# Performance work log

Measured on AMD Instinct MI355X. Metric: run time of the kernel, lower is better.

## Reference

```python
import jax, jax.numpy as jnp
import numpy as np

COND = 128  # mask = first 128 dims are condition (True); last 128 are transformed


def _mlp(h, W1, b1, W2, b2, W3, b3):
    h = jax.nn.relu(h @ W1 + b1)
    h = jax.nn.relu(h @ W2 + b2)
    return h @ W3 + b3


def setup_inputs() -> dict:
    key = jax.random.key(0)
    ks = jax.random.split(key, 8)
    B, D, H, T = 65536, 256, 512, 128
    s = 0.02  # small init so exp(tanh(s_vals)) is well-behaved
    inp = {
        "x": jax.random.normal(ks[0], (B, D), dtype=jnp.float32),
        "Ws1": jax.random.normal(ks[1], (COND, H), dtype=jnp.float32) * s,
        "bs1": jnp.zeros((H,), jnp.float32),
        "Ws2": jax.random.normal(ks[2], (H, H), dtype=jnp.float32) * s,
        "bs2": jnp.zeros((H,), jnp.float32),
        "Ws3": jax.random.normal(ks[3], (H, T), dtype=jnp.float32) * s,
        "bs3": jnp.zeros((T,), jnp.float32),
        "Wt1": jax.random.normal(ks[4], (COND, H), dtype=jnp.float32) * s,
        "bt1": jnp.zeros((H,), jnp.float32),
        "Wt2": jax.random.normal(ks[5], (H, H), dtype=jnp.float32) * s,
        "bt2": jnp.zeros((H,), jnp.float32),
        "Wt3": jax.random.normal(ks[6], (H, T), dtype=jnp.float32) * s,
        "bt3": jnp.zeros((T,), jnp.float32),
    }
    return inp


def reference(x, Ws1, bs1, Ws2, bs2, Ws3, bs3, Wt1, bt1, Wt2, bt2, Wt3, bt3):
    # mask gather: condition = masked dims, transform = the rest
    cond = x[:, :COND]            # [B, COND]
    x_t = x[:, COND:]             # [B, T]
    s_vals = jnp.tanh(_mlp(cond, Ws1, bs1, Ws2, bs2, Ws3, bs3))  # [B, T]
    t_vals = _mlp(cond, Wt1, bt1, Wt2, bt2, Wt3, bt3)            # [B, T]
    y_partial = x_t * jnp.exp(s_vals) + t_vals                   # forward branch (inverse=False)
    log_det = s_vals.sum(axis=1)                                 # [B]
    y = jnp.concatenate([cond, y_partial], axis=1)               # scatter back
    return (y, log_det)
```

## Files before the change

### kernel.cpp

```cpp
#include <hip/hip_runtime.h>
#include <hip/hip_bf16.h>

typedef __bf16          bf16x8_t __attribute__((ext_vector_type(8)));
typedef float           f32x4_t  __attribute__((ext_vector_type(4)));
typedef unsigned short  u16x4_t  __attribute__((ext_vector_type(4)));

#define DIN      256
#define CONDN    128
#define BM       64
#define NTHREADS 512
#define NWAVE    8
#define LDA      136
#define LDH      520

#define OFF_WS1 0
#define OFF_WS2 65536
#define OFF_WS3 327680
#define OFF_WT1 393216
#define OFF_WT2 458752
#define OFF_WT3 720896
#define W_TOTAL 786432

__global__ void prep_w(const float* __restrict__ Ws1, const float* __restrict__ Ws2,
                       const float* __restrict__ Ws3, const float* __restrict__ Wt1,
                       const float* __restrict__ Wt2, const float* __restrict__ Wt3,
                       __hip_bfloat16* __restrict__ wt) {
  int idx = blockIdx.x * blockDim.x + threadIdx.x;
  if (idx >= W_TOTAL) return;
  const float* W; int K, N, off;
  if (idx < OFF_WS2)      { W = Ws1; K = 128; N = 512; off = idx - OFF_WS1; }
  else if (idx < OFF_WS3) { W = Ws2; K = 512; N = 512; off = idx - OFF_WS2; }
  else if (idx < OFF_WT1) { W = Ws3; K = 512; N = 128; off = idx - OFF_WS3; }
  else if (idx < OFF_WT2) { W = Wt1; K = 128; N = 512; off = idx - OFF_WT1; }
  else if (idx < OFF_WT3) { W = Wt2; K = 512; N = 512; off = idx - OFF_WT2; }
  else                    { W = Wt3; K = 512; N = 128; off = idx - OFF_WT3; }
  int n = off / K;
  int k = off - n * K;
  wt[idx] = __float2bfloat16(W[k * N + n]);
}

template<int KTOT, int MT, int NT>
__device__ __forceinline__ void mm_tile(const __hip_bfloat16* __restrict__ Asrc, const int lda,
                                        const __hip_bfloat16* __restrict__ Bsrc,
                                        const int l15, const int l4, f32x4_t acc[MT][NT]) {
  #pragma unroll 4
  for (int kk = 0; kk < KTOT; kk += 32) {
    bf16x8_t a[MT], b[NT];
    #pragma unroll
    for (int m = 0; m < MT; ++m)
      a[m] = *reinterpret_cast<const bf16x8_t*>(&Asrc[(m * 16 + l15) * lda + kk + l4 * 8]);
    #pragma unroll
    for (int n = 0; n < NT; ++n)
      b[n] = *reinterpret_cast<const bf16x8_t*>(&Bsrc[(n * 16 + l15) * KTOT + kk + l4 * 8]);
    #pragma unroll
    for (int m = 0; m < MT; ++m) {
      #pragma unroll
      for (int n = 0; n < NT; ++n)
        acc[m][n] = __builtin_amdgcn_mfma_f32_16x16x32_bf16(a[m], b[n], acc[m][n], 0, 0, 0);
    }
  }
}

template<int MT, int NT>
__device__ __forceinline__ void relu_store(f32x4_t acc[MT][NT], const float* __restrict__ bias,
                                           const int n0, const int l15, const int l4,
                                           __hip_bfloat16* __restrict__ H) {
  #pragma unroll
  for (int n = 0; n < NT; ++n) {
    const float bv = bias[n0 + n * 16 + l15];
    #pragma unroll
    for (int m = 0; m < MT; ++m) {
      #pragma unroll
      for (int r = 0; r < 4; ++r) {
        float v = acc[m][n][r] + bv;
        v = fmaxf(v, 0.0f);
        H[(m * 16 + l4 * 4 + r) * LDH + n0 + n * 16 + l15] = __float2bfloat16(v);
      }
    }
  }
}

#define ZERO_ACC(acc, MT, NT) do {                       \
    _Pragma("unroll") for (int m_ = 0; m_ < MT; ++m_)    \
    _Pragma("unroll") for (int n_ = 0; n_ < NT; ++n_)    \
      acc[m_][n_] = (f32x4_t){0.f, 0.f, 0.f, 0.f};       \
  } while (0)

__global__ __launch_bounds__(NTHREADS, 2)
void realnvp_fused(const float* __restrict__ x, const __hip_bfloat16* __restrict__ wt,
                   const float* __restrict__ bs1, const float* __restrict__ bs2,
                   const float* __restrict__ bs3, const float* __restrict__ bt1,
                   const float* __restrict__ bt2, const float* __restrict__ bt3,
                   float* __restrict__ y, float* __restrict__ ld) {
  __shared__ __hip_bfloat16 sA[BM * LDA];
  __shared__ __hip_bfloat16 sH1[BM * LDH];
  __shared__ __hip_bfloat16 sH2[BM * LDH];
  __shared__ float sLd[NWAVE][BM];

  const int tid  = threadIdx.x;
  const int lane = tid & 63;
  const int wid  = tid >> 6;
  const int l15  = lane & 15;
  const int l4   = lane >> 4;
  const int row0 = blockIdx.x * BM;
  const int n0   = wid * 64;
  const int n3   = wid * 16;

  #pragma unroll
  for (int i = 0; i < 4; ++i) {
    int f = tid + i * NTHREADS;
    int r = f >> 5;
    int c = (f & 31) << 2;
    const float4 v = *reinterpret_cast<const float4*>(&x[(size_t)(row0 + r) * DIN + c]);
    *reinterpret_cast<float4*>(&y[(size_t)(row0 + r) * DIN + c]) = v;
    union { u16x4_t u; __hip_bfloat16 b[4]; } p;
    p.b[0] = __float2bfloat16(v.x); p.b[1] = __float2bfloat16(v.y);
    p.b[2] = __float2bfloat16(v.z); p.b[3] = __float2bfloat16(v.w);
    *reinterpret_cast<u16x4_t*>(&sA[r * LDA + c]) = p.u;
  }
  __syncthreads();

  f32x4_t acc[4][4];
  f32x4_t sfrag[4], tfrag[4];

  ZERO_ACC(acc, 4, 4);
  mm_tile<128, 4, 4>(sA, LDA, wt + OFF_WS1 + (size_t)n0 * 128, l15, l4, acc);
  relu_store<4, 4>(acc, bs1, n0, l15, l4, sH1);
  __syncthreads();
  ZERO_ACC(acc, 4, 4);
  mm_tile<512, 4, 4>(sH1, LDH, wt + OFF_WS2 + (size_t)n0 * 512, l15, l4, acc);
  relu_store<4, 4>(acc, bs2, n0, l15, l4, sH2);
  __syncthreads();
  {
    f32x4_t a3[4][1];
    ZERO_ACC(a3, 4, 1);
    mm_tile<512, 4, 1>(sH2, LDH, wt + OFF_WS3 + (size_t)n3 * 512, l15, l4, a3);
    #pragma unroll
    for (int m = 0; m < 4; ++m) sfrag[m] = a3[m][0];
  }

  ZERO_ACC(acc, 4, 4);
  mm_tile<128, 4, 4>(sA, LDA, wt + OFF_WT1 + (size_t)n0 * 128, l15, l4, acc);
  relu_store<4, 4>(acc, bt1, n0, l15, l4, sH1);
  __syncthreads();
  ZERO_ACC(acc, 4, 4);
  mm_tile<512, 4, 4>(sH1, LDH, wt + OFF_WT2 + (size_t)n0 * 512, l15, l4, acc);
  relu_store<4, 4>(acc, bt2, n0, l15, l4, sH2);
  __syncthreads();
  {
    f32x4_t a3[4][1];
    ZERO_ACC(a3, 4, 1);
    mm_tile<512, 4, 1>(sH2, LDH, wt + OFF_WT3 + (size_t)n3 * 512, l15, l4, a3);
    #pragma unroll
    for (int m = 0; m < 4; ++m) tfrag[m] = a3[m][0];
  }

  const float bsv = bs3[n3 + l15];
  const float btv = bt3[n3 + l15];
  #pragma unroll
  for (int m = 0; m < 4; ++m) {
    #pragma unroll
    for (int r = 0; r < 4; ++r) {
      const int rl   = m * 16 + l4 * 4 + r;
      const int grow = row0 + rl;
      const int col  = n3 + l15;
      float s = tanhf(sfrag[m][r] + bsv);
      float t = tfrag[m][r] + btv;
      float xv = x[(size_t)grow * DIN + CONDN + col];
      y[(size_t)grow * DIN + CONDN + col] = xv * expf(s) + t;
      float ss = s;
      ss += __shfl_xor(ss, 1);
      ss += __shfl_xor(ss, 2);
      ss += __shfl_xor(ss, 4);
      ss += __shfl_xor(ss, 8);
      if (l15 == 0) sLd[wid][rl] = ss;
    }
  }
  __syncthreads();
  if (tid < BM) {
    float v = 0.f;
    #pragma unroll
    for (int w = 0; w < NWAVE; ++w) v += sLd[w][tid];
    ld[row0 + tid] = v;
  }
}

extern "C" void kernel_launch(void* const* d_in, const int* in_sizes, int n_in,
                              void* d_out, int out_size, void* d_ws, size_t ws_size,
                              hipStream_t stream) {
  const float* x   = (const float*)d_in[0];
  const float* Ws1 = (const float*)d_in[1];
  const float* bs1 = (const float*)d_in[2];
  const float* Ws2 = (const float*)d_in[3];
  const float* bs2 = (const float*)d_in[4];
  const float* Ws3 = (const float*)d_in[5];
  const float* bs3 = (const float*)d_in[6];
  const float* Wt1 = (const float*)d_in[7];
  const float* bt1 = (const float*)d_in[8];
  const float* Wt2 = (const float*)d_in[9];
  const float* bt2 = (const float*)d_in[10];
  const float* Wt3 = (const float*)d_in[11];
  const float* bt3 = (const float*)d_in[12];

  const int Btot = in_sizes[0] / DIN;
  float* y  = (float*)d_out;
  float* ld = (float*)d_out + (size_t)Btot * DIN;
  __hip_bfloat16* wt = (__hip_bfloat16*)d_ws;

  prep_w<<<(W_TOTAL + 255) / 256, 256, 0, stream>>>(Ws1, Ws2, Ws3, Wt1, Wt2, Wt3, wt);
  realnvp_fused<<<Btot / BM, NTHREADS, 0, stream>>>(x, wt, bs1, bs2, bs3,
                                                    bt1, bt2, bt3, y, ld);
}
```

Before: 234.0 us.

## Swizzle LDS, merge hidden buffers, prefetch weight fragments, raise occupancy bound

Replaces padded shared-memory layouts with an XOR swizzle and merges the two hidden-activation buffers into one, adding extra barriers so a layer's output can overwrite its input. Weight fragments from global memory are software-prefetched one k-step ahead in registers. The launch bound is raised to request more resident blocks, which shrinks the per-thread register budget and risks spilling the large accumulator arrays.

```diff
diff --git a/kernel.cpp b/kernel.cpp
--- a/kernel.cpp
+++ b/kernel.cpp
@@ -10,8 +10,6 @@
 #define BM       64
 #define NTHREADS 512
 #define NWAVE    8
-#define LDA      136
-#define LDH      520
 
 #define OFF_WS1 0
 #define OFF_WS2 65536
@@ -39,42 +37,56 @@
   wt[idx] = __float2bfloat16(W[k * N + n]);
 }
 
+#define SWZ(row, col) (((((col) >> 3) ^ ((row) & 7)) << 3) + ((col) & 7))
+
 template<int KTOT, int MT, int NT>
-__device__ __forceinline__ void mm_tile(const __hip_bfloat16* __restrict__ Asrc, const int lda,
+__device__ __forceinline__ void mm_tile(const __hip_bfloat16* __restrict__ As, const int lda,
                                         const __hip_bfloat16* __restrict__ Bsrc,
                                         const int l15, const int l4, f32x4_t acc[MT][NT]) {
-  #pragma unroll 4
+  const int xr = l15 & 7;
+  bf16x8_t a[MT], b[NT], bn[NT];
+  #pragma unroll
+  for (int n = 0; n < NT; ++n)
+    b[n] = *reinterpret_cast<const bf16x8_t*>(&Bsrc[(n * 16 + l15) * KTOT + l4 * 8]);
+  #pragma unroll
   for (int kk = 0; kk < KTOT; kk += 32) {
-    bf16x8_t a[MT], b[NT];
+    if (kk + 32 < KTOT) {
+      #pragma unroll
+      for (int n = 0; n < NT; ++n)
+        bn[n] = *reinterpret_cast<const bf16x8_t*>(&Bsrc[(n * 16 + l15) * KTOT + kk + 32 + l4 * 8]);
+    }
     #pragma unroll
     for (int m = 0; m < MT; ++m)
-      a[m] = *reinterpret_cast<const bf16x8_t*>(&Asrc[(m * 16 + l15) * lda + kk + l4 * 8]);
-    #pragma unroll
-    for (int n = 0; n < NT; ++n)
-      b[n] = *reinterpret_cast<const bf16x8_t*>(&Bsrc[(n * 16 + l15) * KTOT + kk + l4 * 8]);
+      a[m] = *reinterpret_cast<const bf16x8_t*>(
+          &As[(m * 16 + l15) * lda + ((((kk >> 3) + l4) ^ xr) << 3)]);
     #pragma unroll
     for (int m = 0; m < MT; ++m) {
       #pragma unroll
       for (int n = 0; n < NT; ++n)
         acc[m][n] = __builtin_amdgcn_mfma_f32_16x16x32_bf16(a[m], b[n], acc[m][n], 0, 0, 0);
     }
-  }
-}
-
-template<int MT, int NT>
+    if (kk + 32 < KTOT) {
+      #pragma unroll
+      for (int n = 0; n < NT; ++n) b[n] = bn[n];
+    }
+  }
+}
+
+template<int MT, int NT, int LD>
 __device__ __forceinline__ void relu_store(f32x4_t acc[MT][NT], const float* __restrict__ bias,
                                            const int n0, const int l15, const int l4,
                                            __hip_bfloat16* __restrict__ H) {
   #pragma unroll
   for (int n = 0; n < NT; ++n) {
-    const float bv = bias[n0 + n * 16 + l15];
+    const int col = n0 + n * 16 + l15;
+    const float bv = bias[col];
     #pragma unroll
     for (int m = 0; m < MT; ++m) {
       #pragma unroll
       for (int r = 0; r < 4; ++r) {
-        float v = acc[m][n][r] + bv;
-        v = fmaxf(v, 0.0f);
-        H[(m * 16 + l4 * 4 + r) * LDH + n0 + n * 16 + l15] = __float2bfloat16(v);
+        const int row = m * 16 + l4 * 4 + r;
+        float v = fmaxf(acc[m][n][r] + bv, 0.0f);
+        H[row * LD + SWZ(row, col)] = __float2bfloat16(v);
       }
     }
   }
@@ -86,16 +98,15 @@
       acc[m_][n_] = (f32x4_t){0.f, 0.f, 0.f, 0.f};       \
   } while (0)
 
-__global__ __launch_bounds__(NTHREADS, 2)
+__global__ __launch_bounds__(NTHREADS, 4)
 void realnvp_fused(const float* __restrict__ x, const __hip_bfloat16* __restrict__ wt,
                    const float* __restrict__ bs1, const float* __restrict__ bs2,
                    const float* __restrict__ bs3, const float* __restrict__ bt1,
                    const float* __restrict__ bt2, const float* __restrict__ bt3,
                    float* __restrict__ y, float* __restrict__ ld) {
-  __shared__ __hip_bfloat16 sA[BM * LDA];
-  __shared__ __hip_bfloat16 sH1[BM * LDH];
-  __shared__ __hip_bfloat16 sH2[BM * LDH];
-  __shared__ float sLd[NWAVE][BM];
+  __shared__ __hip_bfloat16 sA[BM * CONDN];
+  __shared__ __hip_bfloat16 sH[BM * 512];
+  float* sLd = reinterpret_cast<float*>(sA);
 
   const int tid  = threadIdx.x;
   const int lane = tid & 63;
@@ -116,7 +127,7 @@
     union { u16x4_t u; __hip_bfloat16 b[4]; } p;
     p.b[0] = __float2bfloat16(v.x); p.b[1] = __float2bfloat16(v.y);
     p.b[2] = __float2bfloat16(v.z); p.b[3] = __float2bfloat16(v.w);
-    *reinterpret_cast<u16x4_t*>(&sA[r * LDA + c]) = p.u;
+    *reinterpret_cast<u16x4_t*>(&sA[r * CONDN + SWZ(r, c)]) = p.u;
   }
   __syncthreads();
 
@@ -124,33 +135,36 @@
   f32x4_t sfrag[4], tfrag[4];
 
   ZERO_ACC(acc, 4, 4);
-  mm_tile<128, 4, 4>(sA, LDA, wt + OFF_WS1 + (size_t)n0 * 128, l15, l4, acc);
-  relu_store<4, 4>(acc, bs1, n0, l15, l4, sH1);
-  __syncthreads();
-  ZERO_ACC(acc, 4, 4);
-  mm_tile<512, 4, 4>(sH1, LDH, wt + OFF_WS2 + (size_t)n0 * 512, l15, l4, acc);
-  relu_store<4, 4>(acc, bs2, n0, l15, l4, sH2);
+  mm_tile<128, 4, 4>(sA, CONDN, wt + OFF_WS1 + (size_t)n0 * 128, l15, l4, acc);
+  relu_store<4, 4, 512>(acc, bs1, n0, l15, l4, sH);
+  __syncthreads();
+  ZERO_ACC(acc, 4, 4);
+  mm_tile<512, 4, 4>(sH, 512, wt + OFF_WS2 + (size_t)n0 * 512, l15, l4, acc);
+  __syncthreads();
+  relu_store<4, 4, 512>(acc, bs2, n0, l15, l4, sH);
   __syncthreads();
   {
     f32x4_t a3[4][1];
     ZERO_ACC(a3, 4, 1);
-    mm_tile<512, 4, 1>(sH2, LDH, wt + OFF_WS3 + (size_t)n3 * 512, l15, l4, a3);
+    mm_tile<512, 4, 1>(sH, 512, wt + OFF_WS3 + (size_t)n3 * 512, l15, l4, a3);
     #pragma unroll
     for (int m = 0; m < 4; ++m) sfrag[m] = a3[m][0];
   }
-
-  ZERO_ACC(acc, 4, 4);
-  mm_tile<128, 4, 4>(sA, LDA, wt + OFF_WT1 + (size_t)n0 * 128, l15, l4, acc);
-  relu_store<4, 4>(acc, bt1, n0, l15, l4, sH1);
-  __syncthreads();
-  ZERO_ACC(acc, 4, 4);
-  mm_tile<512, 4, 4>(sH1, LDH, wt + OFF_WT2 + (size_t)n0 * 512, l15, l4, acc);
-  relu_store<4, 4>(acc, bt2, n0, l15, l4, sH2);
+  __syncthreads();
+
+  ZERO_ACC(acc, 4, 4);
+  mm_tile<128, 4, 4>(sA, CONDN, wt + OFF_WT1 + (size_t)n0 * 128, l15, l4, acc);
+  relu_store<4, 4, 512>(acc, bt1, n0, l15, l4, sH);
+  __syncthreads();
+  ZERO_ACC(acc, 4, 4);
+  mm_tile<512, 4, 4>(sH, 512, wt + OFF_WT2 + (size_t)n0 * 512, l15, l4, acc);
+  __syncthreads();
+  relu_store<4, 4, 512>(acc, bt2, n0, l15, l4, sH);
   __syncthreads();
   {
     f32x4_t a3[4][1];
     ZERO_ACC(a3, 4, 1);
-    mm_tile<512, 4, 1>(sH2, LDH, wt + OFF_WT3 + (size_t)n3 * 512, l15, l4, a3);
+    mm_tile<512, 4, 1>(sH, 512, wt + OFF_WT3 + (size_t)n3 * 512, l15, l4, a3);
     #pragma unroll
     for (int m = 0; m < 4; ++m) tfrag[m] = a3[m][0];
   }
@@ -173,14 +187,14 @@
       ss += __shfl_xor(ss, 2);
       ss += __shfl_xor(ss, 4);
       ss += __shfl_xor(ss, 8);
-      if (l15 == 0) sLd[wid][rl] = ss;
+      if (l15 == 0) sLd[wid * BM + rl] = ss;
     }
   }
   __syncthreads();
   if (tid < BM) {
     float v = 0.f;
     #pragma unroll
-    for (int w = 0; w < NWAVE; ++w) v += sLd[w][tid];
+    for (int w = 0; w < NWAVE; ++w) v += sLd[w * BM + tid];
     ld[row0 + tid] = v;
   }
 }
```

Result: slower. 330.5 us (+41.3%).
